# Performance work log

Hardware: AMD Instinct MI355X
Metric: run time of the kernel (lower is better)

The kernel has to match this reference:

```python
import jax, jax.numpy as jnp
import numpy as np

N_ATOMS = 64
N_SAMPLES = 2 ** 15
SAMPLERATE = 22050
N_RES = 4096
N_ROOMS = 8
N_COEFFS = N_SAMPLES // 2 + 1


def make_waves():
    # musical_scale_hz(21, 106, 4096//4) -> 4 waveform families (sine, saw, square, triangle)
    n_steps = N_RES // 4
    midi = np.linspace(21.0, 106.0, n_steps)
    f0 = 440.0 * 2.0 ** ((midi - 69.0) / 12.0)
    rps = ((f0 / (SAMPLERATE / 2.0)) * np.pi).astype(np.float32)
    rad = rps[:, None] * np.arange(N_SAMPLES, dtype=np.float32)[None, :]
    sine = np.sin(rad)
    t = rad / (2.0 * np.pi)
    saw = (2.0 * (t - np.floor(t + 0.5))).astype(np.float32)
    sq = np.sign(sine).astype(np.float32)
    tri = (2.0 * np.abs(saw) - 1.0).astype(np.float32)
    return jnp.asarray(np.concatenate([sine, saw, sq, tri], 0).reshape(1, N_RES, N_SAMPLES))


def pdf2(means, stds, n):
    # gaussian pdf evaluated on linspace(0,1,n); means/stds: (1, A)
    rng = jnp.linspace(0.0, 1.0, n)
    mu = means[..., None]
    sd = stds[..., None]
    return jnp.exp(-0.5 * ((rng - mu) / sd) ** 2) / (sd * jnp.sqrt(2.0 * jnp.pi))


def linear_interp(x, n_out):
    # F.interpolate(mode='linear', align_corners=False) on last axis; x: (b, a, f)
    f = x.shape[-1]
    pos = (jnp.arange(n_out) + 0.5) * (f / n_out) - 0.5
    pos = jnp.clip(pos, 0.0, f - 1)
    i0 = jnp.floor(pos).astype(jnp.int32)
    i1 = jnp.minimum(i0 + 1, f - 1)
    w = (pos - i0).astype(x.dtype)
    return x[..., i0] * (1.0 - w) + x[..., i1] * w


def exponential_decay(decay_values, n_atoms, n_frames, base_resonance, n_samples):
    dv = jax.nn.sigmoid(decay_values.reshape(-1, n_atoms, 1))
    dv = jnp.broadcast_to(dv, (dv.shape[0], n_atoms, n_frames))
    decay = base_resonance + dv * (1.0 - base_resonance) * 0.95
    decay = jnp.exp(jnp.cumsum(jnp.log(decay + 1e-12), axis=-1))
    return linear_interp(decay, n_samples)


def fft_convolve(a, b):
    # zero-pad to 2N, multiply spectra, take first N samples
    n = a.shape[-1]
    pa = jnp.pad(a, ((0, 0), (0, 0), (0, n)))
    pb = jnp.pad(b, ((0, 0), (0, 0), (0, n)))
    spec = jnp.fft.rfft(pa, axis=-1) * jnp.fft.rfft(pb, axis=-1)
    return jnp.fft.irfft(spec, n=2 * n, axis=-1)[..., :n]


def layer_norm(x, w, b, eps=1e-5):
    m = jnp.mean(x, axis=-1, keepdims=True)
    v = jnp.var(x, axis=-1, keepdims=True)
    return (x - m) / jnp.sqrt(v + eps) * w + b


def sparse_softmax_st(x):
    soft = jax.nn.softmax(x, axis=-1)
    hard = jax.nn.one_hot(jnp.argmax(x, axis=-1), x.shape[-1], dtype=x.dtype)
    return hard + soft - jax.lax.stop_gradient(soft)


def model_forward(x, mix, decays, filter_decays, resonance_choice, noise_filter,
                  resonance_filter, resonance_filter2, env, amplitudes, verb_params,
                  noise, waves, ln_w, ln_b, mix_w1, mix_w2, room_w1, room_w2, room_irs):
    overall_mix = jax.nn.softmax(mix, axis=-1)                                   # (1,A,2)
    resonances = jnp.einsum('bar,brn->ban', jax.nn.relu(resonance_choice), waves)  # (1,A,N)

    # band-pass filtered noise (gaussian filter in frequency domain)
    noise_spec = jnp.fft.rfft(noise, axis=-1)
    noise_filt = pdf2(noise_filter[:, :, 0], jnp.abs(noise_filter[:, :, 1]) + 1e-12, N_COEFFS)
    filtered_noise = jnp.fft.irfft(noise_spec * noise_filt, n=N_SAMPLES, axis=-1)

    res_spec = jnp.fft.rfft(resonances, axis=-1)
    rf1 = pdf2(jnp.zeros_like(resonance_filter[:, :, 0]),
               jnp.abs(resonance_filter[:, :, 1]) + 1e-12, N_COEFFS)
    filtered_resonance = jnp.fft.irfft(res_spec * rf1, n=N_SAMPLES, axis=-1)
    rf2 = pdf2(jnp.zeros_like(resonance_filter2[:, :, 0]),
               jnp.abs(resonance_filter2[:, :, 1]) + 1e-12, N_COEFFS)
    filt_res_2 = jnp.fft.irfft(res_spec * rf2, n=N_SAMPLES, axis=-1)

    filt_crossfade = exponential_decay(filter_decays, N_ATOMS, 128, 0.02, N_SAMPLES)
    decay_env = exponential_decay(decays, N_ATOMS, 128, 0.02, N_SAMPLES)
    decaying_resonance = filtered_resonance * decay_env
    decaying_resonance2 = filt_res_2 * decay_env

    # gaussian envelope branch (gaussian_envelope = True)
    envelopes = pdf2(env[:, :, 0], jnp.abs(env[:, :, 1] + 1e-12) * 0.1, N_SAMPLES)
    positioned_noise = filtered_noise * envelopes

    res = fft_convolve(positioned_noise, decaying_resonance)
    res2 = fft_convolve(positioned_noise, decaying_resonance2)
    mixed = filt_crossfade * res + (1.0 - filt_crossfade) * res2

    final = positioned_noise * overall_mix[:, :, 0:1] + mixed * overall_mix[:, :, 1:2]
    final = final / (jnp.linalg.norm(final, axis=-1, keepdims=True) + 1e-8)
    amps = jnp.abs(amplitudes)
    final = final * amps

    # ReverbGenerator: layernorm -> small MLPs -> hard room choice -> fft convolve with IR
    h = layer_norm(verb_params, ln_w, ln_b)
    mix_v = jax.nn.sigmoid(jax.nn.leaky_relu(h @ mix_w1) @ mix_w2)               # (1,A,1)
    room_logits = jax.nn.leaky_relu(h @ room_w1) @ room_w2                        # (1,A,R)
    room = sparse_softmax_st(room_logits)
    ir = jnp.einsum('bar,rn->ban', room, room_irs)
    wet = fft_convolve(final, ir)
    out = final * mix_v + wet * (1.0 - mix_v)
    return out, amps


def setup_inputs() -> dict:
    key = jax.random.key(0)
    ks = jax.random.split(key, 20)
    return {
        'x': jax.random.normal(ks[0], (1, 1), jnp.float32),
        'mix': jax.random.uniform(ks[1], (1, N_ATOMS, 2), jnp.float32),
        'decays': jax.random.uniform(ks[2], (1, N_ATOMS, 1), jnp.float32, -6.0, 6.0),
        'filter_decays': jax.random.uniform(ks[3], (1, N_ATOMS, 1), jnp.float32, -6.0, 6.0),
        'resonance_choice': jax.random.uniform(ks[4], (1, N_ATOMS, N_RES), jnp.float32),
        'noise_filter': jax.random.uniform(ks[5], (1, N_ATOMS, 2), jnp.float32),
        'resonance_filter': jax.random.uniform(ks[6], (1, N_ATOMS, 2), jnp.float32),
        'resonance_filter2': jax.random.uniform(ks[7], (1, N_ATOMS, 2), jnp.float32),
        'env': jax.random.uniform(ks[8], (1, N_ATOMS, 2), jnp.float32),
        'amplitudes': jax.random.uniform(ks[9], (1, N_ATOMS, 1), jnp.float32) ** 2,
        'verb_params': jax.random.uniform(ks[10], (1, N_ATOMS, 4), jnp.float32, -1.0, 1.0),
        'noise': jax.random.uniform(ks[11], (1, N_ATOMS, N_SAMPLES), jnp.float32, -1.0, 1.0),
        'waves': make_waves(),
        'ln_w': jnp.ones((4,), jnp.float32),
        'ln_b': jnp.zeros((4,), jnp.float32),
        'mix_w1': jax.random.normal(ks[12], (4, 4), jnp.float32) * 0.1,
        'mix_w2': jax.random.normal(ks[13], (4, 1), jnp.float32) * 0.1,
        'room_w1': jax.random.normal(ks[14], (4, 4), jnp.float32) * 0.1,
        'room_w2': jax.random.normal(ks[15], (4, N_ROOMS), jnp.float32) * 0.1,
        'room_irs': jax.random.normal(ks[16], (N_ROOMS, N_SAMPLES), jnp.float32) * 0.01,
    }


def reference(x, mix, decays, filter_decays, resonance_choice, noise_filter,
              resonance_filter, resonance_filter2, env, amplitudes, verb_params,
              noise, waves, ln_w, ln_b, mix_w1, mix_w2, room_w1, room_w2, room_irs):
    return model_forward(x, mix, decays, filter_decays, resonance_choice, noise_filter,
                         resonance_filter, resonance_filter2, env, amplitudes, verb_params,
                         noise, waves, ln_w, ln_b, mix_w1, mix_w2, room_w1, room_w2, room_irs)
```

## Files before the change

kernel.cpp:

```cpp
#include <hip/hip_runtime.h>


typedef __attribute__((ext_vector_type(8))) short bf16x8;
typedef __attribute__((ext_vector_type(4))) float f32x4;

constexpr int SC_OM0   = 0;
constexpr int SC_OM1   = 64;
constexpr int SC_NFMU  = 128;
constexpr int SC_NFSD  = 192;
constexpr int SC_RF1SD = 256;
constexpr int SC_RF2SD = 320;
constexpr int SC_ENVMU = 384;
constexpr int SC_ENVSD = 448;
constexpr int SC_AMPS  = 512;
constexpr int SC_MIXV  = 576;
constexpr int SC_ROOM  = 832;
constexpr int SC_PSS   = 1024;
constexpr int SC_DTAB  = 4096;
constexpr int SC_FTAB  = 12288;

constexpr size_t OFF_SCAL = 0;
constexpr size_t OFF_CT   = 65536;
constexpr size_t OFF_P    = 327680;
constexpr size_t OFF_DS   = 8716288;
constexpr size_t OFF_RP   = OFF_DS;
constexpr size_t OFF_W64  = 17104896;
constexpr size_t OFF_NSS  = OFF_W64;
constexpr size_t OFF_W2   = OFF_W64 + 4194304;
constexpr size_t OFF_RSS  = 25493504;
constexpr size_t OFF_FINU = OFF_RSS;
constexpr size_t OFF_W1   = 29687808;
constexpr size_t OFF_FN   = 38076416;
constexpr size_t OFF_FR1  = 40173568;
constexpr size_t OFF_FR2  = 42270720;
constexpr size_t OFF_IRS  = 44367872;
constexpr size_t WS_FLOATS= 45416448;

__device__ __forceinline__ float2 cmul(float2 a, float2 b) {
  return make_float2(a.x*b.x - a.y*b.y, a.x*b.y + a.y*b.x);
}

__device__ __forceinline__ short f2bf(float x) {
  unsigned u = __float_as_uint(x);
  u = (u + 0x7FFFu + ((u >> 16) & 1u)) >> 16;
  return (short)u;
}
__device__ __forceinline__ float bf2f(short s) {
  return __uint_as_float((unsigned)(unsigned short)s << 16);
}
__device__ __forceinline__ unsigned pk2(float2 v) {
  return (unsigned)(unsigned short)f2bf(v.x)
       | ((unsigned)(unsigned short)f2bf(v.y) << 16);
}
__device__ __forceinline__ float2 upk2(unsigned u) {
  return make_float2(__uint_as_float(u << 16),
                     __uint_as_float(u & 0xFFFF0000u));
}

__device__ __forceinline__ void dft16(float2 d[16], float ei)
{
  const float CA[4] = {1.0f, 0.92387953251128674f, 0.70710678118654752f, 0.38268343236508977f};
  const float SA[4] = {0.0f, 0.38268343236508977f, 0.70710678118654752f, 0.92387953251128674f};
  const float CB[4] = {1.0f, 0.70710678118654752f, 0.0f, -0.70710678118654752f};
  const float SB[4] = {0.0f, 0.70710678118654752f, 1.0f, 0.70710678118654752f};
  float2 e[16];
  #pragma unroll
  for (int q = 0; q < 4; ++q) {
    float2 x0 = d[q], x1 = d[q+4], x2 = d[q+8], x3 = d[q+12];
    float ca = CA[q], sa = ei*SA[q], cb = CB[q], sb = ei*SB[q];
    float2 sum1 = make_float2(x0.x+x2.x, x0.y+x2.y);
    float2 d1   = make_float2(x0.x-x2.x, x0.y-x2.y);
    float2 dif1 = make_float2(d1.x*ca - d1.y*sa, d1.x*sa + d1.y*ca);
    float2 sum2 = make_float2(x1.x+x3.x, x1.y+x3.y);
    float2 d2   = make_float2(x1.x-x3.x, x1.y-x3.y);
    float2 dt   = make_float2(d2.x*ca - d2.y*sa, d2.x*sa + d2.y*ca);
    float2 dif2 = make_float2(-ei*dt.y, ei*dt.x);
    float2 Dm   = make_float2(sum1.x-sum2.x, sum1.y-sum2.y);
    float2 Dm2  = make_float2(dif1.x-dif2.x, dif1.y-dif2.y);
    e[4*q+0] = make_float2(sum1.x+sum2.x, sum1.y+sum2.y);
    e[4*q+1] = make_float2(dif1.x+dif2.x, dif1.y+dif2.y);
    e[4*q+2] = make_float2(Dm.x*cb - Dm.y*sb, Dm.x*sb + Dm.y*cb);
    e[4*q+3] = make_float2(Dm2.x*cb - Dm2.y*sb, Dm2.x*sb + Dm2.y*cb);
  }
  #pragma unroll
  for (int q = 0; q < 4; ++q) {
    float2 x0 = e[q], x1 = e[q+4], x2 = e[q+8], x3 = e[q+12];
    float2 sum1 = make_float2(x0.x+x2.x, x0.y+x2.y);
    float2 dif1 = make_float2(x0.x-x2.x, x0.y-x2.y);
    float2 sum2 = make_float2(x1.x+x3.x, x1.y+x3.y);
    float2 d2   = make_float2(x1.x-x3.x, x1.y-x3.y);
    float2 dif2 = make_float2(-ei*d2.y, ei*d2.x);
    d[q]    = make_float2(sum1.x+sum2.x, sum1.y+sum2.y);
    d[q+4]  = make_float2(dif1.x+dif2.x, dif1.y+dif2.y);
    d[q+8]  = make_float2(sum1.x-sum2.x, sum1.y-sum2.y);
    d[q+12] = make_float2(dif1.x-dif2.x, dif1.y-dif2.y);
  }
}

__device__ __forceinline__ void twiddleB(float2 d[16], int u, float dir2pi)
{
  float sn1, cs1;
  __sincosf(dir2pi * ((float)u * (1.0f/256.0f)), &sn1, &cs1);
  float2 w1 = make_float2(cs1, sn1);
  float2 tw = w1;
  #pragma unroll
  for (int k = 1; k < 16; ++k) { d[k] = cmul(d[k], tw); tw = cmul(tw, w1); }
}

template<int LEN>
__device__ float2* lds_fft(float2* src, float2* dst,
                           const float2* __restrict__ T256,
                           float dsign, float ei)
{
  constexpr int QB  = LEN >> 2;
  constexpr int FPT = (16 * QB) >> 8;
  constexpr int NST = (LEN == 256) ? 4 : 3;
  int n = LEN, s = 1, ls = 0;
  int sh = (LEN == 256) ? 0 : 1;

  if (LEN == 128) {
    constexpr int HB = LEN >> 1;
    constexpr int BPT = (16 * HB) >> 8;
    __syncthreads();
    #pragma unroll
    for (int b = 0; b < BPT; ++b) {
      int g = threadIdx.x + (b << 8);
      int row = g / HB;
      int beta = g & (HB - 1);
      float2 tj = T256[beta << 1];
      float cs = tj.x, sn = dsign * tj.y;
      float2 av = src[row*LEN + (beta ^ row)];
      float2 bv = src[row*LEN + ((beta + HB) ^ row)];
      float2 sum = make_float2(av.x + bv.x, av.y + bv.y);
      float2 dif = make_float2(av.x - bv.x, av.y - bv.y);
      float2 tw  = make_float2(dif.x*cs - dif.y*sn, dif.x*sn + dif.y*cs);
      dst[row*LEN + ((2*beta)     ^ row)] = sum;
      dst[row*LEN + ((2*beta + 1) ^ row)] = tw;
    }
    float2* t = src; src = dst; dst = t;
    n = 64; s = 2; ls = 1; sh = 2;
  }

  for (int st = 0; st < NST; ++st) {
    __syncthreads();
    #pragma unroll
    for (int b = 0; b < FPT; ++b) {
      int g   = threadIdx.x + (b << 8);
      int row = g / QB;
      int q   = g & (QB - 1);
      int p1  = q >> ls;
      int blo = q & (s - 1);
      int base = row * LEN;
      float2 x0 = src[base + ( q         ^ row)];
      float2 x1 = src[base + ((q +   QB) ^ row)];
      float2 x2 = src[base + ((q + 2*QB) ^ row)];
      float2 x3 = src[base + ((q + 3*QB) ^ row)];
      float2 tA = T256[p1 << sh];
      float caA = tA.x, saA = dsign * tA.y;
      float2 tB = T256[p1 << (sh + 1)];
      float caB = tB.x, saB = dsign * tB.y;
      float2 sum1 = make_float2(x0.x + x2.x, x0.y + x2.y);
      float2 d1   = make_float2(x0.x - x2.x, x0.y - x2.y);
      float2 dif1 = make_float2(d1.x*caA - d1.y*saA, d1.x*saA + d1.y*caA);
      float2 sum2 = make_float2(x1.x + x3.x, x1.y + x3.y);
      float2 d2   = make_float2(x1.x - x3.x, x1.y - x3.y);
      float2 dt   = make_float2(d2.x*caA - d2.y*saA, d2.x*saA + d2.y*caA);
      float2 dif2 = make_float2(-ei * dt.y, ei * dt.x);
      float2 S  = make_float2(sum1.x + sum2.x, sum1.y + sum2.y);
      float2 Dm = make_float2(sum1.x - sum2.x, sum1.y - sum2.y);
      float2 D  = make_float2(Dm.x*caB - Dm.y*saB, Dm.x*saB + Dm.y*caB);
      float2 S2 = make_float2(dif1.x + dif2.x, dif1.y + dif2.y);
      float2 Dm2= make_float2(dif1.x - dif2.x, dif1.y - dif2.y);
      float2 D2 = make_float2(Dm2.x*caB - Dm2.y*saB, Dm2.x*saB + Dm2.y*caB);
      int w0 = (p1 << (ls + 2)) | blo;
      dst[base + ( w0          ^ row)] = S;
      dst[base + ((w0 +     s) ^ row)] = S2;
      dst[base + ((w0 + 2 * s) ^ row)] = D;
      dst[base + ((w0 + 3 * s) ^ row)] = D2;
    }
    float2* t = src; src = dst; dst = t;
    n >>= 2; s <<= 2; ls += 2; sh += 2;
  }
  __syncthreads();
  return src;
}

__global__ __launch_bounds__(256) void k_fft_s256_DsPI(
    unsigned* __restrict__ Ds, unsigned* __restrict__ P,
    unsigned* __restrict__ IRS,
    const float* __restrict__ fr1, const float* __restrict__ fr2,
    const float* __restrict__ fn, const float* __restrict__ rirs,
    const float* __restrict__ scal)
{
  constexpr int N = 65536, NH = 32768;
  constexpr float FWD = -6.283185307179586f;
  __shared__ float2 X[16*16*17];
  __shared__ float2 T256[256];
  __shared__ float2 TN[256];
  const int mode = (blockIdx.y < 64) ? 0 : ((blockIdx.y < 128) ? 1 : 2);
  const int a = (mode == 0) ? blockIdx.y : ((mode == 1) ? blockIdx.y - 64 : blockIdx.y - 128);
  const int n1base = blockIdx.x << 4;
  const int r = threadIdx.x & 15;
  const int u = threadIdx.x >> 4;

  {
    float ang = FWD * ((float)threadIdx.x * (1.0f/256.0f));
    float sn, cs; __sincosf(ang, &sn, &cs);
    T256[threadIdx.x] = make_float2(cs, sn);
    float ang2 = FWD * ((float)threadIdx.x * (1.0f/(float)N));
    float sn2, cs2; __sincosf(ang2, &sn2, &cs2);
    TN[threadIdx.x] = make_float2(cs2, sn2);
  }

  float emu = 0.f, esd = 1.f, egp = 0.f;
  if (mode == 1) {
    emu = scal[SC_ENVMU + a];
    esd = scal[SC_ENVSD + a];
    egp = 0.3989422804014327f / esd;
  }

  float2 d[16];
  #pragma unroll
  for (int m = 0; m < 16; ++m) {
    int j = u + (m << 4);
    int n = n1base + r + 256 * j;
    float2 v = make_float2(0.0f, 0.0f);
    if (n < NH) {
      if (mode == 0) {
        float pos = ((float)n + 0.5f) * (1.0f/256.0f) - 0.5f;
        pos = fminf(fmaxf(pos, 0.0f), 127.0f);
        int i0 = (int)pos;
        float w = pos - (float)i0;
        int i1 = (i0 + 1 < 127) ? i0 + 1 : 127;
        const float* dt = scal + SC_DTAB + a*128;
        float de = dt[i0]*(1.0f-w) + dt[i1]*w;
        v = make_float2(fr1[(size_t)a * NH + n] * de,
                        fr2[(size_t)a * NH + n] * de);
      } else if (mode == 1) {
        float uu = (float)n * (1.0f / 32767.0f);
        float te = (uu - emu) / esd;
        float envv = __expf(-0.5f * te * te) * egp;
        v = make_float2(fn[(size_t)a * NH + n] * envv, 0.0f);
      } else {
        v = make_float2(rirs[(size_t)a * NH + n], 0.0f);
      }
    }
    d[m] = v;
  }

  dft16(d, -1.0f);
  twiddleB(d, u, FWD);
  #pragma unroll
  for (int k = 0; k < 16; ++k) X[(u*16 + k)*17 + r] = d[k];
  __syncthreads();
  #pragma unroll
  for (int m = 0; m < 16; ++m) d[m] = X[(m*16 + u)*17 + r];
  dft16(d, -1.0f);

  unsigned* outp = (mode == 0) ? Ds : ((mode == 1) ? P : IRS);
  #pragma unroll
  for (int k1 = 0; k1 < 16; ++k1) {
    int j = u + (k1 << 4);
    int n = n1base + r + 256 * j;
    int aa = (n1base + r) * j;
    float2 tw = cmul(T256[(aa >> 8) & 255], TN[aa & 255]);
    outp[(size_t)a * N + n] = pk2(cmul(d[k1], tw));
  }
}

__global__ __launch_bounds__(256) void k_fft_s128_first(
    unsigned* __restrict__ RSs, unsigned* __restrict__ NSs,
    const short* __restrict__ rez, const float* __restrict__ noise)
{
  constexpr int N1 = 128, N = 32768;
  constexpr float FWD = -6.283185307179586f;
  __shared__ float2 X[16*16*17];
  __shared__ float2 T256[256];
  __shared__ float2 TN[128];
  const bool isRS = blockIdx.y < 64;
  const int a = isRS ? blockIdx.y : blockIdx.y - 64;
  const int n1base = blockIdx.x << 4;
  const int r = threadIdx.x & 15;
  const int u = threadIdx.x >> 4;

  {
    float ang = FWD * ((float)threadIdx.x * (1.0f/256.0f));
    float sn, cs; __sincosf(ang, &sn, &cs);
    T256[threadIdx.x] = make_float2(cs, sn);
    if (threadIdx.x < 128) {
      float ang2 = FWD * ((float)threadIdx.x * (1.0f/(float)N));
      float sn2, cs2; __sincosf(ang2, &sn2, &cs2);
      TN[threadIdx.x] = make_float2(cs2, sn2);
    }
  }

  float2 d[16];
  #pragma unroll
  for (int m = 0; m < 16; ++m) {
    int j = u + (m << 4);
    int n = n1base + r + N1 * j;
    float x = isRS ? (bf2f(rez[(size_t)a * N + n]) +
                      bf2f(rez[(size_t)(64 + a) * N + n]))
                   : noise[(size_t)a * N + n];
    d[m] = make_float2(x, 0.0f);
  }

  dft16(d, -1.0f);
  twiddleB(d, u, FWD);
  #pragma unroll
  for (int k = 0; k < 16; ++k) X[(u*16 + k)*17 + r] = d[k];
  __syncthreads();
  #pragma unroll
  for (int m = 0; m < 16; ++m) d[m] = X[(m*16 + u)*17 + r];
  dft16(d, -1.0f);

  unsigned* outp = isRS ? RSs : NSs;
  #pragma unroll
  for (int k1 = 0; k1 < 16; ++k1) {
    int j = u + (k1 << 4);
    int n = n1base + r + N1 * j;
    int aa = (n1base + r) * j;
    float2 tw = cmul(T256[(aa >> 7) & 255], TN[aa & 127]);
    outp[(size_t)a * N + n] = pk2(cmul(d[k1], tw));
  }
}

__global__ __launch_bounds__(256) void k_fft_m128_both(
    const unsigned* __restrict__ RSs, const unsigned* __restrict__ NSs,
    unsigned* __restrict__ W1, unsigned* __restrict__ W2,
    const float* __restrict__ scal)
{
  constexpr int N1 = 128;
  constexpr int N = N1 * 256;
  constexpr int ITERS = (16 * N1) >> 8;
  constexpr int LOG2N1 = 7;
  constexpr float FWD = -6.283185307179586f;
  constexpr float IVD = +6.283185307179586f;
  __shared__ float2 A[16 * N1];
  __shared__ float2 B[16 * N1];
  __shared__ float2 T256[256];
  __shared__ float2 TN[N1];
  const bool isRS = blockIdx.y < 64;
  const int a = isRS ? blockIdx.y : blockIdx.y - 64;
  const int colbase = blockIdx.x << 4;

  {
    float ang = FWD * ((float)threadIdx.x * (1.0f/256.0f));
    float sn, cs; __sincosf(ang, &sn, &cs);
    T256[threadIdx.x] = make_float2(cs, sn);
    if (threadIdx.x < N1) {
      float ang2 = IVD * ((float)threadIdx.x * (1.0f/(float)N));
      float sn2, cs2; __sincosf(ang2, &sn2, &cs2);
      TN[threadIdx.x] = make_float2(cs2, sn2);
    }
  }

  float mu = 0.f, isd1 = 0.f, g1 = 0.f, isd2 = 0.f, g2 = 0.f;
  if (isRS) {
    float s1 = scal[SC_RF1SD + a], s2 = scal[SC_RF2SD + a];
    isd1 = 1.0f/s1; g1 = 0.3989422804014327f/s1;
    isd2 = 1.0f/s2; g2 = 0.3989422804014327f/s2;
  } else {
    float sd = scal[SC_NFSD + a]; mu = scal[SC_NFMU + a];
    isd1 = 1.0f/sd; g1 = 0.3989422804014327f/sd;
  }
  const unsigned* zin = (isRS ? RSs : NSs) + (size_t)a * N;
  unsigned* out = (isRS ? W1 : W2) + (size_t)a * N;

  #pragma unroll
  for (int it = 0; it < ITERS; ++it) {
    int flat = threadIdx.x + (it << 8);
    int c = flat / N1, j = flat & (N1 - 1);
    A[c*N1 + (j ^ c)] = upk2(zin[(size_t)(colbase + c) * N1 + j]);
  }
  float2* cur = lds_fft<N1>(A, B, T256, 1.0f, -1.0f);
  float2* alt = (cur == A) ? B : A;

  #pragma unroll
  for (int it = 0; it < ITERS; ++it) {
    int flat = threadIdx.x + (it << 8);
    int c = flat / N1, j = flat & (N1 - 1);
    int idx = c*N1 + (j ^ c);
    float2 v = cur[idx];
    int k  = (colbase + c) + (j << 8);
    int kk = (k <= N - k) ? k : N - k;
    if (isRS) {
      float fr = (float)kk * (2.0f/(float)N);
      float t1 = fr * isd1, t2 = fr * isd2;
      float ga = __expf(-0.5f * t1 * t1) * g1;
      float gb = __expf(-0.5f * t2 * t2) * g2;
      v = make_float2(v.x*ga - v.y*gb, v.x*gb + v.y*ga);
    } else {
      float t = ((float)kk * (2.0f/(float)N) - mu) * isd1;
      float g = __expf(-0.5f * t * t) * g1;
      v.x *= g; v.y *= g;
    }
    cur[idx] = v;
  }

  float2* r2 = lds_fft<N1>(cur, alt, T256, -1.0f, 1.0f);

  #pragma unroll
  for (int it = 0; it < ITERS; ++it) {
    int flat = threadIdx.x + (it << 8);
    int c = flat / N1, j = flat & (N1 - 1);
    float2 v = r2[c*N1 + (j ^ c)];
    int aa = j * (colbase + c);
    float2 t1 = T256[(aa >> LOG2N1) & 255];
    t1.y = -t1.y;
    float2 tw = cmul(t1, TN[aa & (N1 - 1)]);
    out[(size_t)(colbase + c) * N1 + j] = pk2(cmul(v, tw));
  }
}

__global__ __launch_bounds__(256) void k_fft_s128_last(
    const unsigned* __restrict__ W1, const unsigned* __restrict__ W2,
    float* __restrict__ fr1, float* __restrict__ fr2, float* __restrict__ fn)
{
  constexpr int N1 = 128, N = 32768;
  constexpr float IVD = +6.283185307179586f;
  constexpr float S32 = 1.0f / 32768.0f;
  __shared__ float2 X[16*16*17];
  const bool isRS = blockIdx.y < 64;
  const int a = isRS ? blockIdx.y : blockIdx.y - 64;
  const int n1base = blockIdx.x << 4;
  const int r = threadIdx.x & 15;
  const int u = threadIdx.x >> 4;

  const unsigned* cb = (isRS ? W1 : W2) + (size_t)a * N;
  float2 d[16];
  #pragma unroll
  for (int m = 0; m < 16; ++m) {
    int j = u + (m << 4);
    d[m] = upk2(cb[n1base + r + N1 * j]);
  }
  dft16(d, 1.0f);
  twiddleB(d, u, IVD);
  #pragma unroll
  for (int k = 0; k < 16; ++k) X[(u*16 + k)*17 + r] = d[k];
  __syncthreads();
  #pragma unroll
  for (int m = 0; m < 16; ++m) d[m] = X[(m*16 + u)*17 + r];
  dft16(d, 1.0f);

  #pragma unroll
  for (int k1 = 0; k1 < 16; ++k1) {
    int j = u + (k1 << 4);
    int n = n1base + r + N1 * j;
    if (isRS) {
      fr1[(size_t)a * N + n] = d[k1].x * S32;
      fr2[(size_t)a * N + n] = d[k1].y * S32;
    } else {
      fn[(size_t)a * N + n] = d[k1].x * S32;
    }
  }
}

__global__ __launch_bounds__(256) void k_fft_mid256dual(
    const unsigned* __restrict__ zin, const unsigned* __restrict__ zin2half,
    unsigned* __restrict__ out1, const int* __restrict__ roomArr)
{
  constexpr int N = 65536;
  constexpr float FWD = -6.283185307179586f;
  constexpr float IVD = +6.283185307179586f;
  __shared__ float2 X[16*16*17];
  __shared__ float2 T256[256];
  __shared__ float2 TN[256];
  const int a = blockIdx.y;
  const int colbase = blockIdx.x << 4;
  const int u  = threadIdx.x & 15;
  const int rc = threadIdx.x >> 4;

  {
    float ang = FWD * ((float)threadIdx.x * (1.0f/256.0f));
    float sn, cs; __sincosf(ang, &sn, &cs);
    T256[threadIdx.x] = make_float2(cs, sn);
    float ang2 = IVD * ((float)threadIdx.x * (1.0f/(float)N));
    float sn2, cs2; __sincosf(ang2, &sn2, &cs2);
    TN[threadIdx.x] = make_float2(cs2, sn2);
  }
  __syncthreads();

  const unsigned* z2 = zin2half + (size_t)(roomArr ? roomArr[a] : a) * N;
  const size_t rowG = (size_t)a * N + (size_t)(colbase + rc) * 256;
  const size_t rowZ2 = (size_t)(colbase + rc) * 256;

  float2 d[16];
  #pragma unroll
  for (int m = 0; m < 16; ++m) d[m] = upk2(zin[rowG + u + (m << 4)]);
  dft16(d, -1.0f);
  twiddleB(d, u, FWD);
  #pragma unroll
  for (int k = 0; k < 16; ++k) X[(rc*16 + k)*17 + u] = d[k];
  #pragma unroll
  for (int m = 0; m < 16; ++m) d[m] = X[(rc*16 + u)*17 + m];
  dft16(d, -1.0f);

  float2 stash[16];
  #pragma unroll
  for (int k = 0; k < 16; ++k) stash[k] = d[k];
  #pragma unroll
  for (int m = 0; m < 16; ++m) d[m] = upk2(z2[rowZ2 + u + (m << 4)]);
  dft16(d, -1.0f);
  twiddleB(d, u, FWD);
  #pragma unroll
  for (int k = 0; k < 16; ++k) X[(rc*16 + k)*17 + u] = d[k];
  #pragma unroll
  for (int m = 0; m < 16; ++m) d[m] = X[(rc*16 + u)*17 + m];
  dft16(d, -1.0f);
  #pragma unroll
  for (int k = 0; k < 16; ++k) d[k] = cmul(stash[k], d[k]);

  dft16(d, 1.0f);
  twiddleB(d, u, IVD);
  #pragma unroll
  for (int k = 0; k < 16; ++k) X[(rc*16 + k)*17 + u] = d[k];
  #pragma unroll
  for (int m = 0; m < 16; ++m) d[m] = X[(rc*16 + u)*17 + m];
  dft16(d, 1.0f);

  #pragma unroll
  for (int k1 = 0; k1 < 16; ++k1) {
    int j = u + (k1 << 4);
    int aa = j * (colbase + rc);
    float2 t1 = T256[(aa >> 8) & 255];
    t1.y = -t1.y;
    float2 tw = cmul(t1, TN[aa & 255]);
    out1[rowG + j] = pk2(cmul(d[k1], tw));
  }
}

__global__ __launch_bounds__(256) void k_fft_out6fwd(
    const unsigned* __restrict__ W64in, const float* __restrict__ fn,
    float* __restrict__ finU, float* __restrict__ scal,
    unsigned* __restrict__ DsOut)
{
  constexpr int N = 65536, NH = 32768;
  constexpr float FWD = -6.283185307179586f;
  constexpr float IVD = +6.283185307179586f;
  constexpr float S64 = 1.0f / 65536.0f;
  __shared__ float2 X[16*16*17];
  __shared__ float2 T256[256];
  __shared__ float2 TN[256];
  __shared__ float red[256];
  const int a = blockIdx.y;
  const int n1base = blockIdx.x << 4;
  const int r = threadIdx.x & 15;
  const int u = threadIdx.x >> 4;

  {
    float ang = FWD * ((float)threadIdx.x * (1.0f/256.0f));
    float sn, cs; __sincosf(ang, &sn, &cs);
    T256[threadIdx.x] = make_float2(cs, sn);
    float ang2 = FWD * ((float)threadIdx.x * (1.0f/(float)N));
    float sn2, cs2; __sincosf(ang2, &sn2, &cs2);
    TN[threadIdx.x] = make_float2(cs2, sn2);
  }

  const float emu = scal[SC_ENVMU + a];
  const float esd = scal[SC_ENVSD + a];
  const float egp = 0.3989422804014327f / esd;
  const float om0 = scal[SC_OM0 + a], om1 = scal[SC_OM1 + a];
  const float* ft = scal + SC_FTAB + a*128;

  float2 d[16];
  #pragma unroll
  for (int m = 0; m < 16; ++m) {
    int j = u + (m << 4);
    d[m] = upk2(W64in[(size_t)a * N + n1base + r + 256 * j]);
  }
  dft16(d, 1.0f);
  twiddleB(d, u, IVD);
  #pragma unroll
  for (int k = 0; k < 16; ++k) X[(u*16 + k)*17 + r] = d[k];
  __syncthreads();
  #pragma unroll
  for (int m = 0; m < 16; ++m) d[m] = X[(m*16 + u)*17 + r];
  dft16(d, 1.0f);

  float fv[8];
  float ss = 0.0f;
  #pragma unroll
  for (int k1 = 0; k1 < 8; ++k1) {
    int n = n1base + r + 256 * (u + (k1 << 4));
    float resv  = d[k1].x * S64;
    float res2v = d[k1].y * S64;
    float uu = (float)n * (1.0f / 32767.0f);
    float te = (uu - emu) / esd;
    float envv = __expf(-0.5f * te * te) * egp;
    float pnv = fn[(size_t)a * NH + n] * envv;
    float pos = ((float)n + 0.5f) * (1.0f/256.0f) - 0.5f;
    pos = fminf(fmaxf(pos, 0.0f), 127.0f);
    int i0 = (int)pos;
    float w = pos - (float)i0;
    int i1 = (i0 + 1 < 127) ? i0 + 1 : 127;
    float fc = ft[i0]*(1.0f-w) + ft[i1]*w;
    float f = pnv*om0 + (fc*resv + (1.0f-fc)*res2v)*om1;
    finU[(size_t)a * NH + n] = f;
    fv[k1] = f;
    ss += f * f;
  }
  red[threadIdx.x] = ss;
  __syncthreads();
  for (int s = 128; s > 0; s >>= 1) {
    if (threadIdx.x < s) red[threadIdx.x] += red[threadIdx.x + s];
    __syncthreads();
  }
  if (threadIdx.x == 0) scal[SC_PSS + a*16 + blockIdx.x] = red[0];

  #pragma unroll
  for (int m = 0; m < 16; ++m)
    d[m] = (m < 8) ? make_float2(fv[m], 0.0f) : make_float2(0.0f, 0.0f);
  dft16(d, -1.0f);
  twiddleB(d, u, FWD);
  #pragma unroll
  for (int k = 0; k < 16; ++k) X[(u*16 + k)*17 + r] = d[k];
  __syncthreads();
  #pragma unroll
  for (int m = 0; m < 16; ++m) d[m] = X[(m*16 + u)*17 + r];
  dft16(d, -1.0f);

  #pragma unroll
  for (int k1 = 0; k1 < 16; ++k1) {
    int j = u + (k1 << 4);
    int n = n1base + r + 256 * j;
    int aa = (n1base + r) * j;
    float2 tw = cmul(T256[(aa >> 8) & 255], TN[aa & 255]);
    DsOut[(size_t)a * N + n] = pk2(cmul(d[k1], tw));
  }
}

__global__ __launch_bounds__(256) void k_fft_s256_out3(
    const unsigned* __restrict__ W64in, const float* __restrict__ finU,
    const float* __restrict__ scal, float* __restrict__ out)
{
  constexpr int N = 65536, NH = 32768;
  constexpr float IVD = +6.283185307179586f;
  constexpr float S64 = 1.0f / 65536.0f;
  __shared__ float2 X[16*16*17];
  const int a = blockIdx.y;
  const int n1base = blockIdx.x << 4;
  const int r = threadIdx.x & 15;
  const int u = threadIdx.x >> 4;

  float ss = 0.0f;
  #pragma unroll
  for (int i = 0; i < 16; ++i) ss += scal[SC_PSS + a*16 + i];
  float fscale = scal[SC_AMPS + a] / (sqrtf(ss) + 1e-8f);
  float mixv = scal[SC_MIXV + a];
  float w1 = fscale * (1.0f - mixv);
  float w0 = fscale * mixv;

  float2 d[16];
  #pragma unroll
  for (int m = 0; m < 16; ++m) {
    int j = u + (m << 4);
    d[m] = upk2(W64in[(size_t)a * N + n1base + r + 256 * j]);
  }
  dft16(d, 1.0f);
  twiddleB(d, u, IVD);
  #pragma unroll
  for (int k = 0; k < 16; ++k) X[(u*16 + k)*17 + r] = d[k];
  __syncthreads();
  #pragma unroll
  for (int m = 0; m < 16; ++m) d[m] = X[(m*16 + u)*17 + r];
  dft16(d, 1.0f);

  #pragma unroll
  for (int k1 = 0; k1 < 8; ++k1) {
    int n = n1base + r + 256 * (u + (k1 << 4));
    out[(size_t)a * NH + n] =
        d[k1].x * S64 * w1 + finU[(size_t)a * NH + n] * w0;
  }
}

__global__ void k_scalars(
    const float* __restrict__ mix, const float* __restrict__ decays,
    const float* __restrict__ fdec, const float* __restrict__ nf,
    const float* __restrict__ rf1, const float* __restrict__ rf2,
    const float* __restrict__ env, const float* __restrict__ amplitudes,
    const float* __restrict__ verb, const float* __restrict__ ln_w,
    const float* __restrict__ ln_b, const float* __restrict__ mw1,
    const float* __restrict__ mw2, const float* __restrict__ rw1,
    const float* __restrict__ rw2, float* __restrict__ scal,
    float* __restrict__ dout)
{
  int a = threadIdx.x;
  if (a >= 64) return;
  float m0 = mix[a*2+0], m1 = mix[a*2+1];
  float mx = fmaxf(m0, m1);
  float e0 = expf(m0 - mx), e1 = expf(m1 - mx);
  float inv = 1.0f / (e0 + e1);
  scal[SC_OM0+a] = e0 * inv;
  scal[SC_OM1+a] = e1 * inv;
  scal[SC_NFMU+a] = nf[a*2+0];
  scal[SC_NFSD+a] = fabsf(nf[a*2+1]) + 1e-12f;
  scal[SC_RF1SD+a] = fabsf(rf1[a*2+1]) + 1e-12f;
  scal[SC_RF2SD+a] = fabsf(rf2[a*2+1]) + 1e-12f;
  scal[SC_ENVMU+a] = env[a*2+0];
  scal[SC_ENVSD+a] = fabsf(env[a*2+1] + 1e-12f) * 0.1f;
  float amp = fabsf(amplitudes[a]);
  scal[SC_AMPS+a] = amp;
  dout[2097152 + a] = amp;
  float d  = 0.02f + (1.0f/(1.0f+expf(-decays[a]))) * (0.98f * 0.95f);
  float fd = 0.02f + (1.0f/(1.0f+expf(-fdec[a])))   * (0.98f * 0.95f);
  float pd = 1.0f, pf = 1.0f;
  for (int f = 0; f < 128; ++f) {
    pd *= d; pf *= fd;
    scal[SC_DTAB + a*128 + f] = pd;
    scal[SC_FTAB + a*128 + f] = pf;
  }
  float x0 = verb[a*4+0], x1 = verb[a*4+1], x2 = verb[a*4+2], x3 = verb[a*4+3];
  float mean = (x0+x1+x2+x3) * 0.25f;
  float d0 = x0-mean, d1 = x1-mean, d2 = x2-mean, d3 = x3-mean;
  float var = (d0*d0 + d1*d1 + d2*d2 + d3*d3) * 0.25f;
  float rs = 1.0f / sqrtf(var + 1e-5f);
  float h[4] = { d0*rs*ln_w[0]+ln_b[0], d1*rs*ln_w[1]+ln_b[1],
                 d2*rs*ln_w[2]+ln_b[2], d3*rs*ln_w[3]+ln_b[3] };
  float t[4], u[4];
  for (int j = 0; j < 4; ++j) {
    float s1 = 0.f, s2 = 0.f;
    for (int i2 = 0; i2 < 4; ++i2) {
      s1 += h[i2] * mw1[i2*4 + j];
      s2 += h[i2] * rw1[i2*4 + j];
    }
    t[j] = (s1 > 0.f) ? s1 : 0.01f*s1;
    u[j] = (s2 > 0.f) ? s2 : 0.01f*s2;
  }
  float ml = 0.f;
  for (int j = 0; j < 4; ++j) ml += t[j] * mw2[j];
  scal[SC_MIXV+a] = 1.0f / (1.0f + expf(-ml));
  float best = -1e30f; int bi = 0;
  for (int r = 0; r < 8; ++r) {
    float lg = 0.f;
    for (int j = 0; j < 4; ++j) lg += u[j] * rw2[j*8 + r];
    if (lg > best) { best = lg; bi = r; }
  }
  ((int*)scal)[SC_ROOM + a] = bi;
}

__global__ void k_packA(const float* __restrict__ rc, short* __restrict__ ctb)
{
  int o = blockIdx.x * 256 + threadIdx.x;
  int m = o >> 12, k = o & 4095;
  int s = k >> 2, f = k & 3;
  float v = fmaxf(rc[m*4096 + f*1024 + s], 0.0f);
  ctb[o] = f2bf(v);
}

__global__ __launch_bounds__(512) void k_gemm_mfma(
    const float* __restrict__ waves, const short* __restrict__ ctb,
    short* __restrict__ rp)
{
  const int t = threadIdx.x;
  const int w = t >> 6, lane = t & 63;
  const int ml = lane & 15, q = lane >> 4;
  const int col = blockIdx.x * 128 + w * 16 + ml;
  const int part = blockIdx.y;
  const int kb0 = part * 64;

  f32x4 acc[4] = {};

  const float* ws0 = waves + (size_t)(kb0*8 + 2*q) * 32768 + col;
  const float* ws1 = waves + (size_t)(1024 + kb0*8 + 2*q) * 32768 + col;
  const short* abase = ctb + (size_t)ml * 4096 + (size_t)kb0 * 32 + q * 8;

  #define LOADW(v, kbl) { size_t o = (size_t)(kbl) * (8*32768); \
    v[0] = ws0[o]; v[1] = ws0[o + 32768]; v[2] = ws1[o]; v[3] = ws1[o + 32768]; }

  #define DOKB(v, kbl) { \
    float sq0 = (v[0] > 0.f) ? 1.f : ((v[0] < 0.f) ? -1.f : v[0]); \
    float sq1 = (v[1] > 0.f) ? 1.f : ((v[1] < 0.f) ? -1.f : v[1]); \
    float tr0 = 2.f * fabsf(v[2]) - 1.f; \
    float tr1 = 2.f * fabsf(v[3]) - 1.f; \
    bf16x8 b; \
    b[0] = f2bf(v[0]); b[1] = f2bf(v[2]); b[2] = f2bf(sq0); b[3] = f2bf(tr0); \
    b[4] = f2bf(v[1]); b[5] = f2bf(v[3]); b[6] = f2bf(sq1); b[7] = f2bf(tr1); \
    const short* ap = abase + (size_t)(kbl) * 32; \
    acc[0] = __builtin_amdgcn_mfma_f32_16x16x32_bf16(*(const bf16x8*)(ap),                   b, acc[0], 0,0,0); \
    acc[1] = __builtin_amdgcn_mfma_f32_16x16x32_bf16(*(const bf16x8*)(ap + (size_t)16*4096), b, acc[1], 0,0,0); \
    acc[2] = __builtin_amdgcn_mfma_f32_16x16x32_bf16(*(const bf16x8*)(ap + (size_t)32*4096), b, acc[2], 0,0,0); \
    acc[3] = __builtin_amdgcn_mfma_f32_16x16x32_bf16(*(const bf16x8*)(ap + (size_t)48*4096), b, acc[3], 0,0,0); }

  float vA[4], vB[4], vC[4], vD[4];
  LOADW(vA, 0);
  LOADW(vB, 1);
  LOADW(vC, 2);
  LOADW(vD, 3);
  for (int kbl = 0; kbl < 64; kbl += 4) {
    DOKB(vA, kbl);
    if (kbl + 4 < 64) LOADW(vA, kbl + 4);
    DOKB(vB, kbl + 1);
    if (kbl + 5 < 64) LOADW(vB, kbl + 5);
    DOKB(vC, kbl + 2);
    if (kbl + 6 < 64) LOADW(vC, kbl + 6);
    DOKB(vD, kbl + 3);
    if (kbl + 7 < 64) LOADW(vD, kbl + 7);
  }
  #undef LOADW
  #undef DOKB

  #pragma unroll
  for (int mt = 0; mt < 4; ++mt) {
    #pragma unroll
    for (int rr = 0; rr < 4; ++rr) {
      rp[(size_t)(part*64 + mt*16 + q*4 + rr) * 32768 + col] = f2bf(acc[mt][rr]);
    }
  }
}

extern "C" void kernel_launch(void* const* d_in, const int* in_sizes, int n_in,
                              void* d_out, int out_size, void* d_ws, size_t ws_size,
                              hipStream_t stream)
{
  const float* mix   = (const float*)d_in[1];
  const float* dec   = (const float*)d_in[2];
  const float* fdec  = (const float*)d_in[3];
  const float* rc    = (const float*)d_in[4];
  const float* nf    = (const float*)d_in[5];
  const float* rf1   = (const float*)d_in[6];
  const float* rf2   = (const float*)d_in[7];
  const float* env   = (const float*)d_in[8];
  const float* amps  = (const float*)d_in[9];
  const float* verb  = (const float*)d_in[10];
  const float* noise = (const float*)d_in[11];
  const float* waves = (const float*)d_in[12];
  const float* lnw   = (const float*)d_in[13];
  const float* lnb   = (const float*)d_in[14];
  const float* mw1   = (const float*)d_in[15];
  const float* mw2   = (const float*)d_in[16];
  const float* rw1   = (const float*)d_in[17];
  const float* rw2   = (const float*)d_in[18];
  const float* rirs  = (const float*)d_in[19];
  float* out = (float*)d_out;
  float* w   = (float*)d_ws;

  if (ws_size < WS_FLOATS * 4ULL) return;

  float*    scal = w + OFF_SCAL;
  short*    ctb  = (short*)(w + OFF_CT);
  short*    rp   = (short*)(w + OFF_RP);
  unsigned* P    = (unsigned*)(w + OFF_P);
  unsigned* Ds   = (unsigned*)(w + OFF_DS);
  unsigned* W64  = (unsigned*)(w + OFF_W64);
  unsigned* RSs  = (unsigned*)(w + OFF_RSS);
  unsigned* NSs  = (unsigned*)(w + OFF_NSS);
  unsigned* W2   = (unsigned*)(w + OFF_W2);
  float*    finU = w + OFF_FINU;
  unsigned* W1   = (unsigned*)(w + OFF_W1);
  float*    fn   = w + OFF_FN;
  float*    fr1  = w + OFF_FR1;
  float*    fr2  = w + OFF_FR2;
  unsigned* IRS  = (unsigned*)(w + OFF_IRS);
  const int* room = ((const int*)(w + OFF_SCAL)) + SC_ROOM;

  k_scalars<<<1, 64, 0, stream>>>(mix, dec, fdec, nf, rf1, rf2, env, amps, verb,
                                  lnw, lnb, mw1, mw2, rw1, rw2, scal, out);
  k_packA<<<1024, 256, 0, stream>>>(rc, ctb);
  k_gemm_mfma<<<dim3(256, 2), 512, 0, stream>>>(waves, ctb, rp);

  k_fft_s128_first<<<dim3(8,128),256,0,stream>>>(RSs, NSs, rp, noise);
  k_fft_m128_both<<<dim3(16,128),256,0,stream>>>(RSs, NSs, W1, W2, scal);
  k_fft_s128_last<<<dim3(8,128),256,0,stream>>>(W1, W2, fr1, fr2, fn);

  k_fft_s256_DsPI<<<dim3(16,136),256,0,stream>>>(Ds, P, IRS, fr1, fr2, fn, rirs, scal);

  k_fft_mid256dual<<<dim3(16,64),256,0,stream>>>(Ds, P, W64, nullptr);

  k_fft_out6fwd<<<dim3(16,64),256,0,stream>>>(W64, fn, finU, scal, Ds);

  k_fft_mid256dual<<<dim3(16,64),256,0,stream>>>(Ds, IRS, W64, room);

  k_fft_s256_out3<<<dim3(16,64),256,0,stream>>>(W64, finU, scal, out);
}
```

Measured before the change: 293.3 us.

## Store intermediate filtered signals in bf16, fuse scalar kernel, retile GEMM blocks

```diff
diff --git a/kernel.cpp b/kernel.cpp
--- a/kernel.cpp
+++ b/kernel.cpp
@@ -31,8 +31,7 @@
 constexpr size_t OFF_FINU = OFF_RSS;
 constexpr size_t OFF_W1   = 29687808;
 constexpr size_t OFF_FN   = 38076416;
-constexpr size_t OFF_FR1  = 40173568;
-constexpr size_t OFF_FR2  = 42270720;
+constexpr size_t OFF_FRP  = 40173568;
 constexpr size_t OFF_IRS  = 44367872;
 constexpr size_t WS_FLOATS= 45416448;
 
@@ -188,9 +187,8 @@
 __global__ __launch_bounds__(256) void k_fft_s256_DsPI(
     unsigned* __restrict__ Ds, unsigned* __restrict__ P,
     unsigned* __restrict__ IRS,
-    const float* __restrict__ fr1, const float* __restrict__ fr2,
-    const float* __restrict__ fn, const float* __restrict__ rirs,
-    const float* __restrict__ scal)
+    const unsigned* __restrict__ FRP, const short* __restrict__ fnb,
+    const float* __restrict__ rirs, const float* __restrict__ scal)
 {
   constexpr int N = 65536, NH = 32768;
   constexpr float FWD = -6.283185307179586f;
@@ -234,13 +232,13 @@
         int i1 = (i0 + 1 < 127) ? i0 + 1 : 127;
         const float* dt = scal + SC_DTAB + a*128;
         float de = dt[i0]*(1.0f-w) + dt[i1]*w;
-        v = make_float2(fr1[(size_t)a * NH + n] * de,
-                        fr2[(size_t)a * NH + n] * de);
+        float2 fr = upk2(FRP[(size_t)a * NH + n]);
+        v = make_float2(fr.x * de, fr.y * de);
       } else if (mode == 1) {
         float uu = (float)n * (1.0f / 32767.0f);
         float te = (uu - emu) / esd;
         float envv = __expf(-0.5f * te * te) * egp;
-        v = make_float2(fn[(size_t)a * NH + n] * envv, 0.0f);
+        v = make_float2(bf2f(fnb[(size_t)a * NH + n]) * envv, 0.0f);
       } else {
         v = make_float2(rirs[(size_t)a * NH + n], 0.0f);
       }
@@ -415,7 +413,7 @@
 
 __global__ __launch_bounds__(256) void k_fft_s128_last(
     const unsigned* __restrict__ W1, const unsigned* __restrict__ W2,
-    float* __restrict__ fr1, float* __restrict__ fr2, float* __restrict__ fn)
+    unsigned* __restrict__ FRP, short* __restrict__ fnb)
 {
   constexpr int N1 = 128, N = 32768;
   constexpr float IVD = +6.283185307179586f;
@@ -448,10 +446,9 @@
     int j = u + (k1 << 4);
     int n = n1base + r + N1 * j;
     if (isRS) {
-      fr1[(size_t)a * N + n] = d[k1].x * S32;
-      fr2[(size_t)a * N + n] = d[k1].y * S32;
+      FRP[(size_t)a * N + n] = pk2(make_float2(d[k1].x * S32, d[k1].y * S32));
     } else {
-      fn[(size_t)a * N + n] = d[k1].x * S32;
+      fnb[(size_t)a * N + n] = f2bf(d[k1].x * S32);
     }
   }
 }
@@ -531,7 +528,7 @@
 }
 
 __global__ __launch_bounds__(256) void k_fft_out6fwd(
-    const unsigned* __restrict__ W64in, const float* __restrict__ fn,
+    const unsigned* __restrict__ W64in, const short* __restrict__ fnb,
     float* __restrict__ finU, float* __restrict__ scal,
     unsigned* __restrict__ DsOut)
 {
@@ -588,7 +585,7 @@
     float uu = (float)n * (1.0f / 32767.0f);
     float te = (uu - emu) / esd;
     float envv = __expf(-0.5f * te * te) * egp;
-    float pnv = fn[(size_t)a * NH + n] * envv;
+    float pnv = bf2f(fnb[(size_t)a * NH + n]) * envv;
     float pos = ((float)n + 0.5f) * (1.0f/256.0f) - 0.5f;
     pos = fminf(fmaxf(pos, 0.0f), 127.0f);
     int i0 = (int)pos;
@@ -674,7 +671,7 @@
   }
 }
 
-__global__ void k_scalars(
+__global__ void k_packA(const float* __restrict__ rc, short* __restrict__ ctb,
     const float* __restrict__ mix, const float* __restrict__ decays,
     const float* __restrict__ fdec, const float* __restrict__ nf,
     const float* __restrict__ rf1, const float* __restrict__ rf2,
@@ -685,8 +682,15 @@
     const float* __restrict__ rw2, float* __restrict__ scal,
     float* __restrict__ dout)
 {
+  int o = blockIdx.x * 256 + threadIdx.x;
+  {
+    int m = o >> 12, k = o & 4095;
+    int s = k >> 2, f = k & 3;
+    float v = fmaxf(rc[m*4096 + f*1024 + s], 0.0f);
+    ctb[o] = f2bf(v);
+  }
+  if (blockIdx.x != 0 || threadIdx.x >= 64) return;
   int a = threadIdx.x;
-  if (a >= 64) return;
   float m0 = mix[a*2+0], m1 = mix[a*2+1];
   float mx = fmaxf(m0, m1);
   float e0 = expf(m0 - mx), e1 = expf(m1 - mx);
@@ -731,31 +735,22 @@
   for (int j = 0; j < 4; ++j) ml += t[j] * mw2[j];
   scal[SC_MIXV+a] = 1.0f / (1.0f + expf(-ml));
   float best = -1e30f; int bi = 0;
-  for (int r = 0; r < 8; ++r) {
+  for (int rr = 0; rr < 8; ++rr) {
     float lg = 0.f;
-    for (int j = 0; j < 4; ++j) lg += u[j] * rw2[j*8 + r];
-    if (lg > best) { best = lg; bi = r; }
+    for (int j = 0; j < 4; ++j) lg += u[j] * rw2[j*8 + rr];
+    if (lg > best) { best = lg; bi = rr; }
   }
   ((int*)scal)[SC_ROOM + a] = bi;
 }
 
-__global__ void k_packA(const float* __restrict__ rc, short* __restrict__ ctb)
-{
-  int o = blockIdx.x * 256 + threadIdx.x;
-  int m = o >> 12, k = o & 4095;
-  int s = k >> 2, f = k & 3;
-  float v = fmaxf(rc[m*4096 + f*1024 + s], 0.0f);
-  ctb[o] = f2bf(v);
-}
-
-__global__ __launch_bounds__(512) void k_gemm_mfma(
+__global__ __launch_bounds__(256) void k_gemm_mfma(
     const float* __restrict__ waves, const short* __restrict__ ctb,
     short* __restrict__ rp)
 {
   const int t = threadIdx.x;
   const int w = t >> 6, lane = t & 63;
   const int ml = lane & 15, q = lane >> 4;
-  const int col = blockIdx.x * 128 + w * 16 + ml;
+  const int col = blockIdx.x * 64 + w * 16 + ml;
   const int part = blockIdx.y;
   const int kb0 = part * 64;
 
@@ -848,26 +843,25 @@
   unsigned* W2   = (unsigned*)(w + OFF_W2);
   float*    finU = w + OFF_FINU;
   unsigned* W1   = (unsigned*)(w + OFF_W1);
-  float*    fn   = w + OFF_FN;
-  float*    fr1  = w + OFF_FR1;
-  float*    fr2  = w + OFF_FR2;
+  short*    fnb  = (short*)(w + OFF_FN);
+  unsigned* FRP  = (unsigned*)(w + OFF_FRP);
   unsigned* IRS  = (unsigned*)(w + OFF_IRS);
   const int* room = ((const int*)(w + OFF_SCAL)) + SC_ROOM;
 
-  k_scalars<<<1, 64, 0, stream>>>(mix, dec, fdec, nf, rf1, rf2, env, amps, verb,
-                                  lnw, lnb, mw1, mw2, rw1, rw2, scal, out);
-  k_packA<<<1024, 256, 0, stream>>>(rc, ctb);
-  k_gemm_mfma<<<dim3(256, 2), 512, 0, stream>>>(waves, ctb, rp);
+  k_packA<<<1024, 256, 0, stream>>>(rc, ctb, mix, dec, fdec, nf, rf1, rf2, env,
+                                    amps, verb, lnw, lnb, mw1, mw2, rw1, rw2,
+                                    scal, out);
+  k_gemm_mfma<<<dim3(512, 2), 256, 0, stream>>>(waves, ctb, rp);
 
   k_fft_s128_first<<<dim3(8,128),256,0,stream>>>(RSs, NSs, rp, noise);
   k_fft_m128_both<<<dim3(16,128),256,0,stream>>>(RSs, NSs, W1, W2, scal);
-  k_fft_s128_last<<<dim3(8,128),256,0,stream>>>(W1, W2, fr1, fr2, fn);
-
-  k_fft_s256_DsPI<<<dim3(16,136),256,0,stream>>>(Ds, P, IRS, fr1, fr2, fn, rirs, scal);
+  k_fft_s128_last<<<dim3(8,128),256,0,stream>>>(W1, W2, FRP, fnb);
+
+  k_fft_s256_DsPI<<<dim3(16,136),256,0,stream>>>(Ds, P, IRS, FRP, fnb, rirs, scal);
 
   k_fft_mid256dual<<<dim3(16,64),256,0,stream>>>(Ds, P, W64, nullptr);
 
-  k_fft_out6fwd<<<dim3(16,64),256,0,stream>>>(W64, fn, finU, scal, Ds);
+  k_fft_out6fwd<<<dim3(16,64),256,0,stream>>>(W64, fnb, finU, scal, Ds);
 
   k_fft_mid256dual<<<dim3(16,64),256,0,stream>>>(Ds, IRS, W64, room);
 
```

New measurement: 300.3 us. 2.4% more time.
